# Kernel tuning notes

Hardware: AMD Instinct MI355X
Metric: run time of the kernel (lower is better)

Reference implementation:

```python
import jax, jax.numpy as jnp
import numpy as np

B, N, R = 32768, 9, 4
IN_DIM = 5
DIMS = [64, 128, 256]
BN_EPS = 1e-5
LRELU_SLOPE = 0.2


def _rgcn_block(h, adj, ws, wr, b, gamma, beta):
    # Relational GCN: self transform + per-relation aggregation
    hw = jnp.einsum('bnd,rde->brne', h, wr)        # [B,R,N,D]
    agg = jnp.einsum('brmn,brne->bme', adj, hw)    # [B,N,D]
    h = h @ ws + agg + b
    # BatchNorm1d(max_num_atoms): channel axis is the atom index (training-mode batch stats)
    mean = jnp.mean(h, axis=(0, 2), keepdims=True)
    var = jnp.var(h, axis=(0, 2), keepdims=True)
    h = (h - mean) * jax.lax.rsqrt(var + BN_EPS)
    h = h * gamma[None, :, None] + beta[None, :, None]
    # LeakyReLU(0.2)
    return jnp.where(h > 0, h, LRELU_SLOPE * h)


def setup_inputs() -> dict:
    key = jax.random.key(0)
    ks = jax.random.split(key, 10)
    inp = {
        'atom_feats': jax.random.normal(ks[0], (B, N, IN_DIM), jnp.float32),
        'adj': jax.random.uniform(ks[1], (B, R, N, N), jnp.float32),
        'mask': jnp.ones((B, N), jnp.float32),
    }
    dims = [IN_DIM] + DIMS
    for i in range(3):
        din, dout = dims[i], dims[i + 1]
        inp[f'w_self{i}'] = jax.random.normal(ks[2 + 2 * i], (din, dout), jnp.float32) / np.sqrt(din)
        inp[f'w_rel{i}'] = jax.random.normal(ks[3 + 2 * i], (R, din, dout), jnp.float32) / np.sqrt(din)
        inp[f'b{i}'] = jnp.zeros((dout,), jnp.float32)
        inp[f'g{i}'] = jnp.ones((N,), jnp.float32)
        inp[f'be{i}'] = jnp.zeros((N,), jnp.float32)
    inp['fc_w'] = jax.random.normal(ks[8], (DIMS[-1], 1), jnp.float32) / np.sqrt(DIMS[-1])
    inp['fc_b'] = jnp.zeros((1,), jnp.float32)
    return inp


def reference(atom_feats, adj, mask,
              w_self0, w_rel0, b0, g0, be0,
              w_self1, w_rel1, b1, g1, be1,
              w_self2, w_rel2, b2, g2, be2,
              fc_w, fc_b):
    h = atom_feats
    h = _rgcn_block(h, adj, w_self0, w_rel0, b0, g0, be0)
    h = _rgcn_block(h, adj, w_self1, w_rel1, b1, g1, be1)
    h = _rgcn_block(h, adj, w_self2, w_rel2, b2, g2, be2)
    # masked sum readout
    g = jnp.sum(h * mask[:, :, None], axis=1)   # [B,D]
    out = g @ fc_w + fc_b                        # [B,1]
    return out.squeeze(-1)
```

## Files before the change

### kernel.cpp

```cpp
#include <hip/hip_runtime.h>
#include <hip/hip_bf16.h>


#define NB 32768
#define NA 9
#define NR 4
#define D0 5
#define D1 64
#define D2 128
#define D3 256
#define EPS 1e-5f
#define SLOPE 0.2f
#define NSLOT 64
#define YST 56

typedef __hip_bfloat16 bf16;
typedef short bf16x8 __attribute__((ext_vector_type(8)));
typedef float f32x4 __attribute__((ext_vector_type(4)));
typedef float f32x2 __attribute__((ext_vector_type(2)));

__device__ __forceinline__ float bf2f(bf16 v) { return __bfloat162float(v); }
__device__ __forceinline__ bf16  f2bf(float v) { return __float2bfloat16(v); }

__device__ __forceinline__ void cvt8(bf16x8 v, f32x2 out[4]) {
    union { bf16x8 h; unsigned u[4]; } cv; cv.h = v;
    #pragma unroll
    for (int j = 0; j < 4; j++) {
        out[j].x = __uint_as_float(cv.u[j] << 16);
        out[j].y = __uint_as_float(cv.u[j] & 0xffff0000u);
    }
}

__device__ __forceinline__ bf16x8 pack8(const f32x2 y[4]) {
    union { bf16x8 h; unsigned short s[8]; } cv;
    #pragma unroll
    for (int j = 0; j < 4; j++) {
        union { bf16 b; unsigned short s; } t0, t1;
        t0.b = f2bf(y[j].x); t1.b = f2bf(y[j].y);
        cv.s[2*j] = t0.s; cv.s[2*j+1] = t1.s;
    }
    return cv.h;
}

__global__ __launch_bounds__(256) void k_zero(float* __restrict__ hdr, float* __restrict__ out)
{
    int idx = blockIdx.x * 256 + threadIdx.x;
    if (idx < NB) out[idx] = 0.f;
    if (idx < 6240) hdr[idx] = 0.f;
}

template<int DIN, int DOUT>
__global__ __launch_bounds__(256) void k_prep(const float* __restrict__ ws,
                                              const float* __restrict__ wr,
                                              bf16* __restrict__ wt)
{
    constexpr int K5 = 5*DIN;
    int idx = blockIdx.x*256 + threadIdx.x;
    if (idx >= DOUT*K5) return;
    int n = idx / K5, k = idx % K5;
    int s = k / DIN, kk = k % DIN;
    float v = (s == 0) ? ws[(size_t)kk*DOUT + n]
                       : wr[((size_t)(s-1)*DIN + kk)*DOUT + n];
    wt[idx] = f2bf(v);
}

__global__ __launch_bounds__(256) void k_layer0(
    const float* __restrict__ feats, const float* __restrict__ adj,
    const float* __restrict__ ws, const float* __restrict__ wr,
    const float* __restrict__ bias, bf16* __restrict__ hpre, float* __restrict__ slots)
{
    __shared__ float Wsh[5][5][64];
    __shared__ float Bsh[64];
    __shared__ float Adj[4][4][9][9];
    __shared__ float Hsh[4][9][5];
    __shared__ float bstat[18];

    int tid = threadIdx.x;
    int bl  = tid >> 6;
    int e   = tid & 63;
    int b0  = blockIdx.x * 4;

    for (int i = tid; i < 5*64; i += 256) Wsh[0][i/64][i%64] = ws[i];
    for (int i = tid; i < 4*5*64; i += 256) {
        int s = i / 320, rem = i % 320;
        Wsh[1+s][rem/64][rem%64] = wr[i];
    }
    if (tid < 64) Bsh[tid] = bias[tid];
    if (tid < 18) bstat[tid] = 0.f;
    {
        const float* ap = adj + (size_t)(b0 + bl) * (NR*NA*NA);
        float* dst = &Adj[bl][0][0][0];
        for (int i = e; i < NR*NA*NA; i += 64) dst[i] = ap[i];
    }
    {
        const float* fp = feats + (size_t)(b0 + bl) * (NA*D0);
        float* dst = &Hsh[bl][0][0];
        for (int i = e; i < NA*D0; i += 64) dst[i] = fp[i];
    }
    __syncthreads();

    float X[5][9];
    #pragma unroll
    for (int s = 0; s < 5; s++)
        #pragma unroll
        for (int n = 0; n < 9; n++) {
            float a = 0.f;
            #pragma unroll
            for (int k = 0; k < 5; k++) a += Hsh[bl][n][k] * Wsh[s][k][e];
            X[s][n] = a;
        }
    float bv = Bsh[e];
    float out[9];
    #pragma unroll
    for (int m = 0; m < 9; m++) {
        float a = X[0][m] + bv;
        #pragma unroll
        for (int r = 0; r < 4; r++)
            #pragma unroll
            for (int n = 0; n < 9; n++)
                a += Adj[bl][r][m][n] * X[1+r][n];
        out[m] = a;
    }
    bf16* hp = hpre + (size_t)(b0 + bl) * (NA*D1) + e;
    #pragma unroll
    for (int m = 0; m < 9; m++) hp[m*D1] = f2bf(out[m]);

    #pragma unroll
    for (int m = 0; m < 9; m++) {
        float s = out[m], q = out[m]*out[m];
        #pragma unroll
        for (int off = 32; off > 0; off >>= 1) {
            s += __shfl_xor(s, off, 64);
            q += __shfl_xor(q, off, 64);
        }
        if (e == 0) { atomicAdd(&bstat[m], s); atomicAdd(&bstat[9+m], q); }
    }
    __syncthreads();
    if (tid < 9) {
        float* sl = slots + (size_t)(blockIdx.x & (NSLOT-1)) * 32;
        atomicAdd(&sl[tid],      bstat[tid]);
        atomicAdd(&sl[16+tid],   bstat[9+tid]);
    }
}

template<int DOUT>
__global__ void k_finalize(const float* __restrict__ slots,
                           const float* __restrict__ g, const float* __restrict__ be,
                           float* __restrict__ fin)
{
    int n = threadIdx.x;
    if (n < 9) {
        float s = 0.f, q = 0.f;
        for (int i = 0; i < NSLOT; i++) { s += slots[i*32+n]; q += slots[i*32+16+n]; }
        float cnt = (float)NB * (float)DOUT;
        float mean = s / cnt;
        float var  = q / cnt - mean*mean;
        float sc   = g[n] * rsqrtf(var + EPS);
        fin[n]    = sc;
        fin[16+n] = be[n] - mean * sc;
    }
}

template<int DIN, int DOUT, int MODE>
__global__ __launch_bounds__(256, 3) void k_mfma(
    const bf16*  __restrict__ hprev,
    const float* __restrict__ finPrev,
    const float* __restrict__ adjg,
    const bf16*  __restrict__ wt,
    const float* __restrict__ bias,
    bf16*  __restrict__ hout,
    float* __restrict__ slots,
    const float* __restrict__ finC,
    const float* __restrict__ maskg,
    const float* __restrict__ fcw,
    float* __restrict__ outp)
{
    constexpr int K5 = 5*DIN;
    constexpr int HS = DIN + 8;
    constexpr int NT = DOUT/64;
    constexpr int KS = DIN/32;
    constexpr int HW8 = DIN/8;

    __shared__ __align__(16) bf16 hS[81*HS];
    __shared__ __align__(16) bf16 yS[4*64*YST];
    __shared__ float rstat[128];
    __shared__ float sfinP[32];
    __shared__ float sfinC[32];

    int tid = threadIdx.x;
    int row0 = blockIdx.x * 64;
    int mol_lo = row0 / 9;
    int mol_hi = (row0 + 63) / 9;
    int nmol = mol_hi - mol_lo + 1;
    int off = row0 - mol_lo*9;

    if (tid < 32) sfinP[tid] = finPrev[tid];
    if constexpr (MODE == 2) { if (tid >= 32 && tid < 64) sfinC[tid-32] = finC[tid-32]; }
    if (tid >= 64 && tid < 192) rstat[tid-64] = 0.f;

    int brow = tid >> 2;
    int bc8  = (tid & 3) * 8;
    int bloc = off + brow;
    int bml  = bloc / 9;
    int ba   = bloc - bml*9;
    float adjR[4][9];
    {
        const float* ap = adjg + (size_t)(mol_lo + bml)*324 + ba*9;
        #pragma unroll
        for (int r = 0; r < 4; r++)
            #pragma unroll
            for (int n = 0; n < 9; n++) adjR[r][n] = ap[r*81 + n];
    }
    __syncthreads();

    for (int i = tid; i < nmol*9*HW8; i += 256) {
        int rl = i / HW8;
        int a  = rl % 9;
        int c8 = (i % HW8)*8;
        bf16x8 hv = *(const bf16x8*)(hprev + (size_t)(mol_lo*9 + rl)*DIN + c8);
        f32x2 hf[4]; cvt8(hv, hf);
        float sc = sfinP[a], sh = sfinP[16+a];
        f32x2 o[4];
        #pragma unroll
        for (int j = 0; j < 4; j++) {
            float v0 = sc*hf[j].x + sh; v0 = fmaxf(v0, SLOPE*v0);
            float v1 = sc*hf[j].y + sh; v1 = fmaxf(v1, SLOPE*v1);
            o[j] = (f32x2){v0, v1};
        }
        *(bf16x8*)(&hS[rl*HS + c8]) = pack8(o);
    }
    __syncthreads();

    int wv = tid >> 6, lane = tid & 63;
    int q = lane >> 4, l15 = lane & 15;

    f32x4 acc[4][NT];
    #pragma unroll
    for (int mt = 0; mt < 4; mt++)
        #pragma unroll
        for (int t = 0; t < NT; t++) acc[mt][t] = (f32x4){0.f, 0.f, 0.f, 0.f};

    const bf16* wp[NT];
    #pragma unroll
    for (int t = 0; t < NT; t++)
        wp[t] = wt + (size_t)((wv*NT + t)*16 + l15)*K5 + q*8;

    #pragma unroll
    for (int ks = 0; ks < KS; ks++) {
        bf16x8 Af[4], Bf[NT];
        #pragma unroll
        for (int mt = 0; mt < 4; mt++)
            Af[mt] = *(const bf16x8*)(hS + (size_t)(off + mt*16 + l15)*HS + ks*32 + q*8);
        #pragma unroll
        for (int t = 0; t < NT; t++)
            Bf[t] = *(const bf16x8*)(wp[t] + ks*32);
        #pragma unroll
        for (int mt = 0; mt < 4; mt++)
            #pragma unroll
            for (int t = 0; t < NT; t++)
                acc[mt][t] = __builtin_amdgcn_mfma_f32_16x16x32_bf16(Af[mt], Bf[t], acc[mt][t], 0, 0, 0);
    }

    for (int kc = 0; kc < KS; kc++) {
        {
            const bf16* hb = hS + (size_t)(bml*9)*HS + kc*32 + bc8;
            f32x2 y[4][4];
            #pragma unroll
            for (int r = 0; r < 4; r++)
                #pragma unroll
                for (int j = 0; j < 4; j++) y[r][j] = (f32x2){0.f, 0.f};
            #pragma unroll
            for (int n = 0; n < 9; n++) {
                bf16x8 hv = *(const bf16x8*)(hb + n*HS);
                f32x2 hf[4]; cvt8(hv, hf);
                #pragma unroll
                for (int r = 0; r < 4; r++) {
                    f32x2 av = (f32x2){adjR[r][n], adjR[r][n]};
                    #pragma unroll
                    for (int j = 0; j < 4; j++)
                        y[r][j] = __builtin_elementwise_fma(av, hf[j], y[r][j]);
                }
            }
            #pragma unroll
            for (int r = 0; r < 4; r++)
                *(bf16x8*)(&yS[(r*64 + brow)*YST + bc8]) = pack8(y[r]);
        }
        __syncthreads();
        #pragma unroll
        for (int r = 0; r < 4; r++) {
            int kcol = DIN + (r*KS + kc)*32;
            bf16x8 Af[4], Bf[NT];
            #pragma unroll
            for (int mt = 0; mt < 4; mt++)
                Af[mt] = *(const bf16x8*)(&yS[(r*64 + mt*16 + l15)*YST + q*8]);
            #pragma unroll
            for (int t = 0; t < NT; t++)
                Bf[t] = *(const bf16x8*)(wp[t] + kcol);
            #pragma unroll
            for (int mt = 0; mt < 4; mt++)
                #pragma unroll
                for (int t = 0; t < NT; t++)
                    acc[mt][t] = __builtin_amdgcn_mfma_f32_16x16x32_bf16(Af[mt], Bf[t], acc[mt][t], 0, 0, 0);
        }
        __syncthreads();
    }

    float bcol[NT];
    #pragma unroll
    for (int t = 0; t < NT; t++) bcol[t] = bias[(wv*NT + t)*16 + l15];

    if constexpr (MODE == 2) {
        float fwv[NT];
        #pragma unroll
        for (int t = 0; t < NT; t++) fwv[t] = fcw[(wv*NT + t)*16 + l15];
        #pragma unroll
        for (int mt = 0; mt < 4; mt++) {
            #pragma unroll
            for (int reg = 0; reg < 4; reg++) {
                int rloc = mt*16 + q*4 + reg;
                int atom = (row0 + rloc) % 9;
                float sc = sfinC[atom], sh = sfinC[16+atom];
                float part = 0.f;
                #pragma unroll
                for (int t = 0; t < NT; t++) {
                    float v = acc[mt][t][reg] + bcol[t];
                    float y = sc*v + sh;
                    y = fmaxf(y, SLOPE*y);
                    part += y * fwv[t];
                }
                part += __shfl_xor(part, 1); part += __shfl_xor(part, 2);
                part += __shfl_xor(part, 4); part += __shfl_xor(part, 8);
                if (l15 == 0) atomicAdd(&rstat[rloc], part);
            }
        }
        __syncthreads();
        if (tid < 64) {
            int rg = row0 + tid;
            int b = rg / 9;
            atomicAdd(&outp[b], rstat[tid] * maskg[rg]);
        }
        return;
    }

    #pragma unroll
    for (int mt = 0; mt < 4; mt++) {
        #pragma unroll
        for (int reg = 0; reg < 4; reg++) {
            int rloc = mt*16 + q*4 + reg;
            float s = 0.f, qq = 0.f;
            #pragma unroll
            for (int t = 0; t < NT; t++) {
                float v = acc[mt][t][reg] + bcol[t];
                if constexpr (MODE == 0) {
                    size_t o = (size_t)(row0 + rloc)*DOUT + (wv*NT + t)*16 + l15;
                    hout[o] = f2bf(v);
                }
                s += v; qq += v*v;
            }
            s += __shfl_xor(s, 1); s += __shfl_xor(s, 2);
            s += __shfl_xor(s, 4); s += __shfl_xor(s, 8);
            qq += __shfl_xor(qq, 1); qq += __shfl_xor(qq, 2);
            qq += __shfl_xor(qq, 4); qq += __shfl_xor(qq, 8);
            if (l15 == 0) { atomicAdd(&rstat[rloc*2], s); atomicAdd(&rstat[rloc*2+1], qq); }
        }
    }
    __syncthreads();
    if (tid < 64) {
        int rg = row0 + tid;
        int atom = rg % 9;
        float* sl = slots + (size_t)(blockIdx.x & (NSLOT-1))*32;
        atomicAdd(&sl[atom],    rstat[tid*2]);
        atomicAdd(&sl[16+atom], rstat[tid*2+1]);
    }
}

__global__ __launch_bounds__(256) void k_readout(
    const bf16* __restrict__ h2, const float* __restrict__ fin,
    const float* __restrict__ mask, const float* __restrict__ fcw,
    const float* __restrict__ fcb, float* __restrict__ out)
{
    int tid = threadIdx.x;
    int w = tid >> 6, lane = tid & 63;
    int b = blockIdx.x * 4 + w;
    float sc[9], sh[9];
    #pragma unroll
    for (int n = 0; n < 9; n++) { sc[n] = fin[n]; sh[n] = fin[16+n]; }
    const bf16* hp = h2 + (size_t)b * (NA*D3) + lane*4;
    float acc0 = 0.f, acc1 = 0.f, acc2 = 0.f, acc3 = 0.f;
    #pragma unroll
    for (int n = 0; n < 9; n++) {
        bf16 v4[4] __attribute__((aligned(8)));
        *(uint2*)v4 = *(const uint2*)(hp + n*D3);
        float mk = mask[(size_t)b*NA + n];
        float v;
        v = sc[n]*bf2f(v4[0]) + sh[n]; v = fmaxf(v, SLOPE*v); acc0 += v*mk;
        v = sc[n]*bf2f(v4[1]) + sh[n]; v = fmaxf(v, SLOPE*v); acc1 += v*mk;
        v = sc[n]*bf2f(v4[2]) + sh[n]; v = fmaxf(v, SLOPE*v); acc2 += v*mk;
        v = sc[n]*bf2f(v4[3]) + sh[n]; v = fmaxf(v, SLOPE*v); acc3 += v*mk;
    }
    float4 wv = *(const float4*)(fcw + lane*4);
    float s = acc0*wv.x + acc1*wv.y + acc2*wv.z + acc3*wv.w;
    #pragma unroll
    for (int off = 1; off < 64; off <<= 1) s += __shfl_xor(s, off, 64);
    if (lane == 0) out[b] = s + fcb[0];
}

__global__ __launch_bounds__(256) void k_addfcb(float* __restrict__ out, const float* __restrict__ fcb)
{
    int idx = blockIdx.x * 256 + threadIdx.x;
    if (idx < NB) out[idx] += fcb[0];
}


extern "C" void kernel_launch(void* const* d_in, const int* in_sizes, int n_in,
                              void* d_out, int out_size, void* d_ws, size_t ws_size,
                              hipStream_t stream)
{
    const float* feats = (const float*)d_in[0];
    const float* adj   = (const float*)d_in[1];
    const float* mask  = (const float*)d_in[2];
    const float* ws0 = (const float*)d_in[3];
    const float* wr0 = (const float*)d_in[4];
    const float* b0  = (const float*)d_in[5];
    const float* g0  = (const float*)d_in[6];
    const float* be0 = (const float*)d_in[7];
    const float* ws1 = (const float*)d_in[8];
    const float* wr1 = (const float*)d_in[9];
    const float* b1  = (const float*)d_in[10];
    const float* g1  = (const float*)d_in[11];
    const float* be1 = (const float*)d_in[12];
    const float* ws2 = (const float*)d_in[13];
    const float* wr2 = (const float*)d_in[14];
    const float* b2  = (const float*)d_in[15];
    const float* g2  = (const float*)d_in[16];
    const float* be2 = (const float*)d_in[17];
    const float* fcw = (const float*)d_in[18];
    const float* fcb = (const float*)d_in[19];
    float* outp = (float*)d_out;

    char* wsb = (char*)d_ws;
    float* slots0 = (float*)(wsb + 0);
    float* slots1 = slots0 + NSLOT*32;
    float* slots2 = slots1 + NSLOT*32;
    float* fin0 = (float*)(wsb + 24576);
    float* fin1 = fin0 + 32;
    float* fin2 = fin1 + 32;
    bf16* wt1 = (bf16*)(wsb + 32768);
    bf16* wt2 = (bf16*)(wsb + 114688);

    k_zero<<<(NB+255)/256, 256, 0, stream>>>((float*)wsb, outp);
    k_prep<D1, D2><<<(D2*5*D1 + 255)/256, 256, 0, stream>>>(ws1, wr1, wt1);
    k_prep<D2, D3><<<(D3*5*D2 + 255)/256, 256, 0, stream>>>(ws2, wr2, wt2);

    bool bigws = (ws_size >= 227016704ULL);
    const int GRID = (NB*NA)/64;

    if (bigws) {
        bf16* h1 = (bf16*)(wsb + 524288ULL);
        bf16* h2 = (bf16*)(wsb + 76021760ULL);
        bf16* h0 = h2;

        k_layer0<<<NB/4, 256, 0, stream>>>(feats, adj, ws0, wr0, b0, h0, slots0);
        k_finalize<D1><<<1, 64, 0, stream>>>(slots0, g0, be0, fin0);

        k_mfma<D1, D2, 0><<<GRID, 256, 0, stream>>>(
            h0, fin0, adj, wt1, b1, h1, slots1, nullptr, nullptr, nullptr, nullptr);
        k_finalize<D2><<<1, 64, 0, stream>>>(slots1, g1, be1, fin1);

        k_mfma<D2, D3, 0><<<GRID, 256, 0, stream>>>(
            h1, fin1, adj, wt2, b2, h2, slots2, nullptr, nullptr, nullptr, nullptr);
        k_finalize<D3><<<1, 64, 0, stream>>>(slots2, g2, be2, fin2);

        k_readout<<<NB/4, 256, 0, stream>>>(h2, fin2, mask, fcw, fcb, outp);
    } else {
        bf16* h0 = (bf16*)(wsb + 524288ULL);
        bf16* h1 = (bf16*)(wsb + 38273024ULL);

        k_layer0<<<NB/4, 256, 0, stream>>>(feats, adj, ws0, wr0, b0, h0, slots0);
        k_finalize<D1><<<1, 64, 0, stream>>>(slots0, g0, be0, fin0);

        k_mfma<D1, D2, 0><<<GRID, 256, 0, stream>>>(
            h0, fin0, adj, wt1, b1, h1, slots1, nullptr, nullptr, nullptr, nullptr);
        k_finalize<D2><<<1, 64, 0, stream>>>(slots1, g1, be1, fin1);

        k_mfma<D2, D3, 1><<<GRID, 256, 0, stream>>>(
            h1, fin1, adj, wt2, b2, nullptr, slots2, nullptr, nullptr, nullptr, nullptr);
        k_finalize<D3><<<1, 64, 0, stream>>>(slots2, g2, be2, fin2);

        k_mfma<D2, D3, 2><<<GRID, 256, 0, stream>>>(
            h1, fin1, adj, wt2, b2, nullptr, nullptr, fin2, mask, fcw, outp);
        k_addfcb<<<(NB+255)/256, 256, 0, stream>>>(outp, fcb);
    }
}
```

Measured before the change: 704.4 us.

## Reorder RGCN layers to transform-then-aggregate with MFMA adjacency and deterministic stats

The fused layer kernel now computes H·W_s and H·W_r for every relation with MFMA first, then aggregates per molecule with a second MFMA against a padded bf16 adjacency tile. Blocks cover 5 molecules and a 64-column output slice on a 2D grid, so atom rows are aligned to molecule boundaries. BatchNorm statistics move out of atomics into separate k_stats / finalize2 reduction kernels, and the readout writes per-column-block partials that are summed afterwards. This removes atomic contention and the scalar adjacency FMA pass, at the cost of redundant adjacency staging per column block, extra passes over activations for stats, and lower occupancy.

```diff
diff --git a/kernel.cpp b/kernel.cpp
--- a/kernel.cpp
+++ b/kernel.cpp
@@ -11,8 +11,9 @@
 #define D3 256
 #define EPS 1e-5f
 #define SLOPE 0.2f
-#define NSLOT 64
-#define YST 56
+#define NMOL 5
+#define MR 48
+#define NBLK ((NB + NMOL - 1) / NMOL)
 
 typedef __hip_bfloat16 bf16;
 typedef short bf16x8 __attribute__((ext_vector_type(8)));
@@ -21,6 +22,9 @@
 
 __device__ __forceinline__ float bf2f(bf16 v) { return __bfloat162float(v); }
 __device__ __forceinline__ bf16  f2bf(float v) { return __float2bfloat16(v); }
+__device__ __forceinline__ short f2bfs(float v) {
+    union { bf16 b; short s; } u; u.b = __float2bfloat16(v); return u.s;
+}
 
 __device__ __forceinline__ void cvt8(bf16x8 v, f32x2 out[4]) {
     union { bf16x8 h; unsigned u[4]; } cv; cv.h = v;
@@ -42,38 +46,30 @@
     return cv.h;
 }
 
-__global__ __launch_bounds__(256) void k_zero(float* __restrict__ hdr, float* __restrict__ out)
-{
-    int idx = blockIdx.x * 256 + threadIdx.x;
-    if (idx < NB) out[idx] = 0.f;
-    if (idx < 6240) hdr[idx] = 0.f;
-}
-
 template<int DIN, int DOUT>
 __global__ __launch_bounds__(256) void k_prep(const float* __restrict__ ws,
                                               const float* __restrict__ wr,
                                               bf16* __restrict__ wt)
 {
-    constexpr int K5 = 5*DIN;
     int idx = blockIdx.x*256 + threadIdx.x;
-    if (idx >= DOUT*K5) return;
-    int n = idx / K5, k = idx % K5;
-    int s = k / DIN, kk = k % DIN;
-    float v = (s == 0) ? ws[(size_t)kk*DOUT + n]
-                       : wr[((size_t)(s-1)*DIN + kk)*DOUT + n];
+    if (idx >= 5*DOUT*DIN) return;
+    int s = idx / (DOUT*DIN);
+    int rem = idx % (DOUT*DIN);
+    int n = rem / DIN, k = rem % DIN;
+    float v = (s == 0) ? ws[(size_t)k*DOUT + n]
+                       : wr[((size_t)(s-1)*DIN + k)*DOUT + n];
     wt[idx] = f2bf(v);
 }
 
 __global__ __launch_bounds__(256) void k_layer0(
     const float* __restrict__ feats, const float* __restrict__ adj,
     const float* __restrict__ ws, const float* __restrict__ wr,
-    const float* __restrict__ bias, bf16* __restrict__ hpre, float* __restrict__ slots)
+    const float* __restrict__ bias, bf16* __restrict__ hpre)
 {
     __shared__ float Wsh[5][5][64];
     __shared__ float Bsh[64];
     __shared__ float Adj[4][4][9][9];
     __shared__ float Hsh[4][9][5];
-    __shared__ float bstat[18];
 
     int tid = threadIdx.x;
     int bl  = tid >> 6;
@@ -86,7 +82,6 @@
         Wsh[1+s][rem/64][rem%64] = wr[i];
     }
     if (tid < 64) Bsh[tid] = bias[tid];
-    if (tid < 18) bstat[tid] = 0.f;
     {
         const float* ap = adj + (size_t)(b0 + bl) * (NR*NA*NA);
         float* dst = &Adj[bl][0][0][0];
@@ -110,7 +105,7 @@
             X[s][n] = a;
         }
     float bv = Bsh[e];
-    float out[9];
+    bf16* hp = hpre + (size_t)(b0 + bl) * (NA*D1) + e;
     #pragma unroll
     for (int m = 0; m < 9; m++) {
         float a = X[0][m] + bv;
@@ -119,39 +114,52 @@
             #pragma unroll
             for (int n = 0; n < 9; n++)
                 a += Adj[bl][r][m][n] * X[1+r][n];
-        out[m] = a;
-    }
-    bf16* hp = hpre + (size_t)(b0 + bl) * (NA*D1) + e;
-    #pragma unroll
-    for (int m = 0; m < 9; m++) hp[m*D1] = f2bf(out[m]);
-
-    #pragma unroll
-    for (int m = 0; m < 9; m++) {
-        float s = out[m], q = out[m]*out[m];
-        #pragma unroll
-        for (int off = 32; off > 0; off >>= 1) {
-            s += __shfl_xor(s, off, 64);
-            q += __shfl_xor(q, off, 64);
-        }
-        if (e == 0) { atomicAdd(&bstat[m], s); atomicAdd(&bstat[9+m], q); }
-    }
+        hp[m*D1] = f2bf(a);
+    }
+}
+
+template<int D>
+__global__ __launch_bounds__(256) void k_stats(const bf16* __restrict__ h,
+                                               float2* __restrict__ sbuf)
+{
+    int g = blockIdx.x;
+    int a = blockIdx.y;
+    int tid = threadIdx.x;
+    constexpr int NIT = (512*D/8)/256;
+    const bf16* base = h + ((size_t)g*512*NA + a)*D;
+    float s = 0.f, q = 0.f;
+    for (int it = 0; it < NIT; it++) {
+        int i = (it*256 + tid)*8;
+        int b = i / D, c = i % D;
+        bf16x8 hv = *(const bf16x8*)(base + (size_t)b*NA*D + c);
+        f32x2 hf[4]; cvt8(hv, hf);
+        #pragma unroll
+        for (int j = 0; j < 4; j++) {
+            s += hf[j].x + hf[j].y;
+            q += hf[j].x*hf[j].x + hf[j].y*hf[j].y;
+        }
+    }
+    #pragma unroll
+    for (int off = 1; off < 64; off <<= 1) {
+        s += __shfl_xor(s, off, 64);
+        q += __shfl_xor(q, off, 64);
+    }
+    __shared__ float ls[4], lq[4];
+    if ((tid & 63) == 0) { ls[tid >> 6] = s; lq[tid >> 6] = q; }
     __syncthreads();
-    if (tid < 9) {
-        float* sl = slots + (size_t)(blockIdx.x & (NSLOT-1)) * 32;
-        atomicAdd(&sl[tid],      bstat[tid]);
-        atomicAdd(&sl[16+tid],   bstat[9+tid]);
-    }
+    if (tid == 0)
+        sbuf[a*64 + g] = (float2){ls[0]+ls[1]+ls[2]+ls[3], lq[0]+lq[1]+lq[2]+lq[3]};
 }
 
 template<int DOUT>
-__global__ void k_finalize(const float* __restrict__ slots,
+__global__ void k_finalize(const float2* __restrict__ sbuf,
                            const float* __restrict__ g, const float* __restrict__ be,
                            float* __restrict__ fin)
 {
     int n = threadIdx.x;
     if (n < 9) {
         float s = 0.f, q = 0.f;
-        for (int i = 0; i < NSLOT; i++) { s += slots[i*32+n]; q += slots[i*32+16+n]; }
+        for (int i = 0; i < 64; i++) { float2 v = sbuf[n*64 + i]; s += v.x; q += v.y; }
         float cnt = (float)NB * (float)DOUT;
         float mean = s / cnt;
         float var  = q / cnt - mean*mean;
@@ -161,216 +169,279 @@
     }
 }
 
+__global__ __launch_bounds__(256) void k_finalize2(
+    const float* __restrict__ pbS, const float* __restrict__ pbQ,
+    const float* __restrict__ g, const float* __restrict__ be, float* __restrict__ fin)
+{
+    int a = blockIdx.x;
+    int tid = threadIdx.x;
+    float s = 0.f, q = 0.f;
+    for (int i = tid; i < NBLK*4; i += 256) { s += pbS[(size_t)i*16 + a]; q += pbQ[(size_t)i*16 + a]; }
+    #pragma unroll
+    for (int off = 1; off < 64; off <<= 1) {
+        s += __shfl_xor(s, off, 64);
+        q += __shfl_xor(q, off, 64);
+    }
+    __shared__ float ls[4], lq[4];
+    if ((tid & 63) == 0) { ls[tid >> 6] = s; lq[tid >> 6] = q; }
+    __syncthreads();
+    if (tid == 0) {
+        float S = ls[0]+ls[1]+ls[2]+ls[3];
+        float Q = lq[0]+lq[1]+lq[2]+lq[3];
+        float cnt = (float)NB * (float)D3;
+        float mean = S / cnt;
+        float var  = Q / cnt - mean*mean;
+        float sc   = g[a] * rsqrtf(var + EPS);
+        fin[a]    = sc;
+        fin[16+a] = be[a] - mean * sc;
+    }
+}
+
 template<int DIN, int DOUT, int MODE>
-__global__ __launch_bounds__(256, 3) void k_mfma(
+__global__ __launch_bounds__(256, 2) void k_fused(
     const bf16*  __restrict__ hprev,
     const float* __restrict__ finPrev,
     const float* __restrict__ adjg,
     const bf16*  __restrict__ wt,
     const float* __restrict__ bias,
     bf16*  __restrict__ hout,
-    float* __restrict__ slots,
+    float* __restrict__ pbS,
+    float* __restrict__ pbQ,
     const float* __restrict__ finC,
     const float* __restrict__ maskg,
     const float* __restrict__ fcw,
-    float* __restrict__ outp)
-{
-    constexpr int K5 = 5*DIN;
-    constexpr int HS = DIN + 8;
-    constexpr int NT = DOUT/64;
-    constexpr int KS = DIN/32;
+    float* __restrict__ out4)
+{
+    constexpr int HSP = DIN + 8;
+    constexpr int SRP = 80;
+    constexpr int XTP = 4*SRP + 8;
+    constexpr int AP  = 72;
+    constexpr int KK1 = DIN/32;
     constexpr int HW8 = DIN/8;
 
-    __shared__ __align__(16) bf16 hS[81*HS];
-    __shared__ __align__(16) bf16 yS[4*64*YST];
-    __shared__ float rstat[128];
+    __shared__ __align__(16) bf16  hS[MR*HSP];
+    __shared__ __align__(16) short xT[64*XTP];
+    __shared__ __align__(16) bf16  adjB[NMOL*16*AP];
+    __shared__ float aggL[64*45];
+    __shared__ float wsumS[4*48], wsumQ[4*48];
+    __shared__ float rowS[48], rowQ[48];
     __shared__ float sfinP[32];
-    __shared__ float sfinC[32];
+    __shared__ float sfinC2[32];
 
     int tid = threadIdx.x;
-    int row0 = blockIdx.x * 64;
-    int mol_lo = row0 / 9;
-    int mol_hi = (row0 + 63) / 9;
-    int nmol = mol_hi - mol_lo + 1;
-    int off = row0 - mol_lo*9;
-
-    if (tid < 32) sfinP[tid] = finPrev[tid];
-    if constexpr (MODE == 2) { if (tid >= 32 && tid < 64) sfinC[tid-32] = finC[tid-32]; }
-    if (tid >= 64 && tid < 192) rstat[tid-64] = 0.f;
-
-    int brow = tid >> 2;
-    int bc8  = (tid & 3) * 8;
-    int bloc = off + brow;
-    int bml  = bloc / 9;
-    int ba   = bloc - bml*9;
-    float adjR[4][9];
-    {
-        const float* ap = adjg + (size_t)(mol_lo + bml)*324 + ba*9;
-        #pragma unroll
-        for (int r = 0; r < 4; r++)
-            #pragma unroll
-            for (int n = 0; n < 9; n++) adjR[r][n] = ap[r*81 + n];
+    int lane = tid & 63;
+    int wv = tid >> 6;
+    int mol_lo = blockIdx.x * NMOL;
+    int nmol = NB - mol_lo; if (nmol > NMOL) nmol = NMOL;
+    int nrow = nmol * 9;
+    int cb = blockIdx.y * 64;
+
+    if (lane < 32) sfinP[lane] = finPrev[lane];
+    if constexpr (MODE == 2) { if (lane >= 32) sfinC2[lane-32] = finC[lane-32]; }
+
+    const bf16x8 z8 = (bf16x8){0,0,0,0,0,0,0,0};
+
+    for (int i = tid; i < 64*XTP/8; i += 256) ((bf16x8*)xT)[i] = z8;
+
+    for (int i = tid; i < MR*HW8; i += 256) {
+        int rl = i / HW8;
+        int c8 = (i % HW8)*8;
+        bf16x8 o8 = z8;
+        if (rl < nrow) {
+            bf16x8 hv = *(const bf16x8*)(hprev + (size_t)(mol_lo*9 + rl)*DIN + c8);
+            f32x2 hf[4]; cvt8(hv, hf);
+            int a = rl % 9;
+            float sc = sfinP[a], sh = sfinP[16+a];
+            f32x2 o[4];
+            #pragma unroll
+            for (int j = 0; j < 4; j++) {
+                float v0 = sc*hf[j].x + sh; v0 = fmaxf(v0, SLOPE*v0);
+                float v1 = sc*hf[j].y + sh; v1 = fmaxf(v1, SLOPE*v1);
+                o[j] = (f32x2){v0, v1};
+            }
+            o8 = pack8(o);
+        }
+        *(bf16x8*)(&hS[rl*HSP + c8]) = o8;
+    }
+
+    for (int i = tid; i < NMOL*7*(AP/8); i += 256) {
+        int molm = i / (AP/8);
+        int c8 = (i % (AP/8))*8;
+        int mol = molm / 7, m = 9 + molm % 7;
+        *(bf16x8*)(&adjB[(mol*16 + m)*AP + c8]) = z8;
+    }
+    for (int i = tid; i < NMOL*9*4*7; i += 256) {
+        int mol = i / 252;
+        int t = i % 252;
+        int m = t / 28;
+        int u = t % 28;
+        int r = u / 7, n = 9 + u % 7;
+        adjB[(mol*16 + m)*AP + 16*r + n] = f2bf(0.f);
+    }
+    for (int i = tid; i < nmol*324; i += 256) {
+        int mol = i / 324;
+        int t = i % 324;
+        int r = t / 81;
+        int m = (t % 81) / 9;
+        int n = t % 9;
+        float v = adjg[(size_t)(mol_lo + mol)*324 + t];
+        adjB[(mol*16 + m)*AP + 16*r + n] = f2bf(v);
     }
     __syncthreads();
 
-    for (int i = tid; i < nmol*9*HW8; i += 256) {
-        int rl = i / HW8;
-        int a  = rl % 9;
-        int c8 = (i % HW8)*8;
-        bf16x8 hv = *(const bf16x8*)(hprev + (size_t)(mol_lo*9 + rl)*DIN + c8);
-        f32x2 hf[4]; cvt8(hv, hf);
-        float sc = sfinP[a], sh = sfinP[16+a];
-        f32x2 o[4];
-        #pragma unroll
-        for (int j = 0; j < 4; j++) {
-            float v0 = sc*hf[j].x + sh; v0 = fmaxf(v0, SLOPE*v0);
-            float v1 = sc*hf[j].y + sh; v1 = fmaxf(v1, SLOPE*v1);
-            o[j] = (f32x2){v0, v1};
-        }
-        *(bf16x8*)(&hS[rl*HS + c8]) = pack8(o);
-    }
-    __syncthreads();
-
-    int wv = tid >> 6, lane = tid & 63;
     int q = lane >> 4, l15 = lane & 15;
-
-    f32x4 acc[4][NT];
-    #pragma unroll
-    for (int mt = 0; mt < 4; mt++)
-        #pragma unroll
-        for (int t = 0; t < NT; t++) acc[mt][t] = (f32x4){0.f, 0.f, 0.f, 0.f};
-
-    const bf16* wp[NT];
-    #pragma unroll
-    for (int t = 0; t < NT; t++)
-        wp[t] = wt + (size_t)((wv*NT + t)*16 + l15)*K5 + q*8;
-
-    #pragma unroll
-    for (int ks = 0; ks < KS; ks++) {
-        bf16x8 Af[4], Bf[NT];
-        #pragma unroll
-        for (int mt = 0; mt < 4; mt++)
-            Af[mt] = *(const bf16x8*)(hS + (size_t)(off + mt*16 + l15)*HS + ks*32 + q*8);
-        #pragma unroll
-        for (int t = 0; t < NT; t++)
-            Bf[t] = *(const bf16x8*)(wp[t] + ks*32);
-        #pragma unroll
-        for (int mt = 0; mt < 4; mt++)
-            #pragma unroll
-            for (int t = 0; t < NT; t++)
-                acc[mt][t] = __builtin_amdgcn_mfma_f32_16x16x32_bf16(Af[mt], Bf[t], acc[mt][t], 0, 0, 0);
-    }
-
-    for (int kc = 0; kc < KS; kc++) {
+    int wl = wv*16 + l15;
+    int wcol = cb + wl;
+
+    f32x4 accS[3];
+    f32x4 accR[4][3];
+    #pragma unroll
+    for (int mt = 0; mt < 3; mt++) accS[mt] = (f32x4){0.f,0.f,0.f,0.f};
+    #pragma unroll
+    for (int s = 0; s < 4; s++)
+        #pragma unroll
+        for (int mt = 0; mt < 3; mt++) accR[s][mt] = (f32x4){0.f,0.f,0.f,0.f};
+
+    const bf16* wbase = wt + (size_t)wcol*DIN + q*8;
+    #pragma unroll
+    for (int kk = 0; kk < KK1; kk++) {
+        bf16x8 Af[3];
+        #pragma unroll
+        for (int mt = 0; mt < 3; mt++)
+            Af[mt] = *(const bf16x8*)(&hS[(mt*16 + l15)*HSP + kk*32 + q*8]);
         {
-            const bf16* hb = hS + (size_t)(bml*9)*HS + kc*32 + bc8;
-            f32x2 y[4][4];
-            #pragma unroll
-            for (int r = 0; r < 4; r++)
-                #pragma unroll
-                for (int j = 0; j < 4; j++) y[r][j] = (f32x2){0.f, 0.f};
-            #pragma unroll
-            for (int n = 0; n < 9; n++) {
-                bf16x8 hv = *(const bf16x8*)(hb + n*HS);
-                f32x2 hf[4]; cvt8(hv, hf);
-                #pragma unroll
-                for (int r = 0; r < 4; r++) {
-                    f32x2 av = (f32x2){adjR[r][n], adjR[r][n]};
-                    #pragma unroll
-                    for (int j = 0; j < 4; j++)
-                        y[r][j] = __builtin_elementwise_fma(av, hf[j], y[r][j]);
+            bf16x8 Bf = *(const bf16x8*)(wbase + kk*32);
+            #pragma unroll
+            for (int mt = 0; mt < 3; mt++)
+                accS[mt] = __builtin_amdgcn_mfma_f32_16x16x32_bf16(Af[mt], Bf, accS[mt], 0, 0, 0);
+        }
+        #pragma unroll
+        for (int s = 0; s < 4; s++) {
+            bf16x8 Bf = *(const bf16x8*)(wbase + (size_t)(s+1)*DOUT*DIN + kk*32);
+            #pragma unroll
+            for (int mt = 0; mt < 3; mt++)
+                accR[s][mt] = __builtin_amdgcn_mfma_f32_16x16x32_bf16(Af[mt], Bf, accR[s][mt], 0, 0, 0);
+        }
+    }
+    short* xcol = xT + (size_t)wl*XTP;
+    #pragma unroll
+    for (int s = 0; s < 4; s++)
+        #pragma unroll
+        for (int mt = 0; mt < 3; mt++)
+            #pragma unroll
+            for (int reg = 0; reg < 4; reg++) {
+                int row = mt*16 + q*4 + reg;
+                if (row < 45) {
+                    int mu = row / 9, n = row % 9;
+                    xcol[s*SRP + mu*16 + n] = f2bfs(accR[s][mt][reg]);
                 }
             }
-            #pragma unroll
-            for (int r = 0; r < 4; r++)
-                *(bf16x8*)(&yS[(r*64 + brow)*YST + bc8]) = pack8(y[r]);
+
+    f32x4 accA[NMOL];
+    for (int mu = 0; mu < nmol; mu++) {
+        f32x4 acc = (f32x4){0.f,0.f,0.f,0.f};
+        #pragma unroll
+        for (int kk = 0; kk < 2; kk++) {
+            int k0 = kk*32 + q*8;
+            int rr = k0 >> 4;
+            int n0 = k0 & 15;
+            bf16x8 Af = *(const bf16x8*)(&adjB[((mu*16) + l15)*AP + k0]);
+            bf16x8 Bf = *(const bf16x8*)(&xcol[rr*SRP + mu*16 + n0]);
+            acc = __builtin_amdgcn_mfma_f32_16x16x32_bf16(Af, Bf, acc, 0, 0, 0);
+        }
+        accA[mu] = acc;
+    }
+    for (int mu = 0; mu < nmol; mu++) {
+        #pragma unroll
+        for (int reg = 0; reg < 4; reg++) {
+            int atom = q*4 + reg;
+            if (atom < 9) aggL[wl*45 + mu*9 + atom] = accA[mu][reg];
+        }
+    }
+
+    float bcol = bias[wcol];
+
+    if constexpr (MODE == 0) {
+        #pragma unroll
+        for (int mt = 0; mt < 3; mt++) {
+            #pragma unroll
+            for (int reg = 0; reg < 4; reg++) {
+                int row = mt*16 + q*4 + reg;
+                if (row < nrow) {
+                    float v = accS[mt][reg] + aggL[wl*45 + row] + bcol;
+                    hout[(size_t)(mol_lo*9 + row)*DOUT + wcol] = f2bf(v);
+                }
+            }
+        }
+        return;
+    }
+
+    if constexpr (MODE == 1) {
+        #pragma unroll
+        for (int mt = 0; mt < 3; mt++) {
+            #pragma unroll
+            for (int reg = 0; reg < 4; reg++) {
+                int row = mt*16 + q*4 + reg;
+                float s = 0.f, qq = 0.f;
+                if (row < nrow) {
+                    float v = accS[mt][reg] + aggL[wl*45 + row] + bcol;
+                    s = v; qq = v*v;
+                }
+                s += __shfl_xor(s, 1); s += __shfl_xor(s, 2);
+                s += __shfl_xor(s, 4); s += __shfl_xor(s, 8);
+                qq += __shfl_xor(qq, 1); qq += __shfl_xor(qq, 2);
+                qq += __shfl_xor(qq, 4); qq += __shfl_xor(qq, 8);
+                if (l15 == 0) { wsumS[wv*48 + row] = s; wsumQ[wv*48 + row] = qq; }
+            }
         }
         __syncthreads();
-        #pragma unroll
-        for (int r = 0; r < 4; r++) {
-            int kcol = DIN + (r*KS + kc)*32;
-            bf16x8 Af[4], Bf[NT];
-            #pragma unroll
-            for (int mt = 0; mt < 4; mt++)
-                Af[mt] = *(const bf16x8*)(&yS[(r*64 + mt*16 + l15)*YST + q*8]);
-            #pragma unroll
-            for (int t = 0; t < NT; t++)
-                Bf[t] = *(const bf16x8*)(wp[t] + kcol);
-            #pragma unroll
-            for (int mt = 0; mt < 4; mt++)
-                #pragma unroll
-                for (int t = 0; t < NT; t++)
-                    acc[mt][t] = __builtin_amdgcn_mfma_f32_16x16x32_bf16(Af[mt], Bf[t], acc[mt][t], 0, 0, 0);
+        if (tid < 48) {
+            rowS[tid] = wsumS[tid] + wsumS[48+tid] + wsumS[96+tid] + wsumS[144+tid];
+            rowQ[tid] = wsumQ[tid] + wsumQ[48+tid] + wsumQ[96+tid] + wsumQ[144+tid];
         }
         __syncthreads();
-    }
-
-    float bcol[NT];
-    #pragma unroll
-    for (int t = 0; t < NT; t++) bcol[t] = bias[(wv*NT + t)*16 + l15];
-
-    if constexpr (MODE == 2) {
-        float fwv[NT];
-        #pragma unroll
-        for (int t = 0; t < NT; t++) fwv[t] = fcw[(wv*NT + t)*16 + l15];
-        #pragma unroll
-        for (int mt = 0; mt < 4; mt++) {
+        if (tid < 9) {
+            float sA = 0.f, qA = 0.f;
+            #pragma unroll
+            for (int mu = 0; mu < NMOL; mu++) { sA += rowS[mu*9 + tid]; qA += rowQ[mu*9 + tid]; }
+            size_t pi = ((size_t)blockIdx.y*NBLK + blockIdx.x)*16 + tid;
+            pbS[pi] = sA;
+            pbQ[pi] = qA;
+        }
+        return;
+    }
+
+    {
+        float fw = fcw[wcol];
+        #pragma unroll
+        for (int mt = 0; mt < 3; mt++) {
             #pragma unroll
             for (int reg = 0; reg < 4; reg++) {
-                int rloc = mt*16 + q*4 + reg;
-                int atom = (row0 + rloc) % 9;
-                float sc = sfinC[atom], sh = sfinC[16+atom];
+                int row = mt*16 + q*4 + reg;
                 float part = 0.f;
-                #pragma unroll
-                for (int t = 0; t < NT; t++) {
-                    float v = acc[mt][t][reg] + bcol[t];
-                    float y = sc*v + sh;
+                if (row < nrow) {
+                    int atom = row % 9;
+                    float v = accS[mt][reg] + aggL[wl*45 + row] + bcol;
+                    float y = sfinC2[atom]*v + sfinC2[16+atom];
                     y = fmaxf(y, SLOPE*y);
-                    part += y * fwv[t];
+                    part = y * fw;
                 }
                 part += __shfl_xor(part, 1); part += __shfl_xor(part, 2);
                 part += __shfl_xor(part, 4); part += __shfl_xor(part, 8);
-                if (l15 == 0) atomicAdd(&rstat[rloc], part);
+                if (l15 == 0) wsumS[wv*48 + row] = part;
             }
         }
         __syncthreads();
-        if (tid < 64) {
-            int rg = row0 + tid;
-            int b = rg / 9;
-            atomicAdd(&outp[b], rstat[tid] * maskg[rg]);
-        }
-        return;
-    }
-
-    #pragma unroll
-    for (int mt = 0; mt < 4; mt++) {
-        #pragma unroll
-        for (int reg = 0; reg < 4; reg++) {
-            int rloc = mt*16 + q*4 + reg;
-            float s = 0.f, qq = 0.f;
-            #pragma unroll
-            for (int t = 0; t < NT; t++) {
-                float v = acc[mt][t][reg] + bcol[t];
-                if constexpr (MODE == 0) {
-                    size_t o = (size_t)(row0 + rloc)*DOUT + (wv*NT + t)*16 + l15;
-                    hout[o] = f2bf(v);
-                }
-                s += v; qq += v*v;
-            }
-            s += __shfl_xor(s, 1); s += __shfl_xor(s, 2);
-            s += __shfl_xor(s, 4); s += __shfl_xor(s, 8);
-            qq += __shfl_xor(qq, 1); qq += __shfl_xor(qq, 2);
-            qq += __shfl_xor(qq, 4); qq += __shfl_xor(qq, 8);
-            if (l15 == 0) { atomicAdd(&rstat[rloc*2], s); atomicAdd(&rstat[rloc*2+1], qq); }
-        }
-    }
-    __syncthreads();
-    if (tid < 64) {
-        int rg = row0 + tid;
-        int atom = rg % 9;
-        float* sl = slots + (size_t)(blockIdx.x & (NSLOT-1))*32;
-        atomicAdd(&sl[atom],    rstat[tid*2]);
-        atomicAdd(&sl[16+atom], rstat[tid*2+1]);
+        if (tid < nrow)
+            rowS[tid] = (wsumS[tid] + wsumS[48+tid] + wsumS[96+tid] + wsumS[144+tid])
+                        * maskg[(size_t)mol_lo*9 + tid];
+        __syncthreads();
+        if (tid < nmol) {
+            float t = 0.f;
+            #pragma unroll
+            for (int j = 0; j < 9; j++) t += rowS[tid*9 + j];
+            out4[(size_t)blockIdx.y*NB + mol_lo + tid] = t;
+        }
     }
 }
 
@@ -398,17 +469,20 @@
         v = sc[n]*bf2f(v4[2]) + sh[n]; v = fmaxf(v, SLOPE*v); acc2 += v*mk;
         v = sc[n]*bf2f(v4[3]) + sh[n]; v = fmaxf(v, SLOPE*v); acc3 += v*mk;
     }
-    float4 wv = *(const float4*)(fcw + lane*4);
-    float s = acc0*wv.x + acc1*wv.y + acc2*wv.z + acc3*wv.w;
+    float4 wvv = *(const float4*)(fcw + lane*4);
+    float s = acc0*wvv.x + acc1*wvv.y + acc2*wvv.z + acc3*wvv.w;
     #pragma unroll
     for (int off = 1; off < 64; off <<= 1) s += __shfl_xor(s, off, 64);
     if (lane == 0) out[b] = s + fcb[0];
 }
 
-__global__ __launch_bounds__(256) void k_addfcb(float* __restrict__ out, const float* __restrict__ fcb)
+__global__ __launch_bounds__(256) void k_sum4(float* __restrict__ out,
+                                              const float* __restrict__ out4,
+                                              const float* __restrict__ fcb)
 {
     int idx = blockIdx.x * 256 + threadIdx.x;
-    if (idx < NB) out[idx] += fcb[0];
+    if (idx < NB)
+        out[idx] = out4[idx] + out4[NB+idx] + out4[2*NB+idx] + out4[3*NB+idx] + fcb[0];
 }
 
 
@@ -439,56 +513,65 @@
     float* outp = (float*)d_out;
 
     char* wsb = (char*)d_ws;
-    float* slots0 = (float*)(wsb + 0);
-    float* slots1 = slots0 + NSLOT*32;
-    float* slots2 = slots1 + NSLOT*32;
-    float* fin0 = (float*)(wsb + 24576);
+    float2* sbuf0 = (float2*)(wsb + 0);
+    float2* sbuf1 = sbuf0 + 576;
+    float2* sbuf2 = sbuf1 + 576;
+    float* fin0 = (float*)(wsb + 16384);
     float* fin1 = fin0 + 32;
     float* fin2 = fin1 + 32;
     bf16* wt1 = (bf16*)(wsb + 32768);
     bf16* wt2 = (bf16*)(wsb + 114688);
-
-    k_zero<<<(NB+255)/256, 256, 0, stream>>>((float*)wsb, outp);
-    k_prep<D1, D2><<<(D2*5*D1 + 255)/256, 256, 0, stream>>>(ws1, wr1, wt1);
-    k_prep<D2, D3><<<(D3*5*D2 + 255)/256, 256, 0, stream>>>(ws2, wr2, wt2);
-
-    bool bigws = (ws_size >= 227016704ULL);
-    const int GRID = (NB*NA)/64;
+    float* out4 = (float*)(wsb + 442368);
+    float* pbS  = (float*)(wsb + 966656);
+    float* pbQ  = (float*)(wsb + 2644480);
+
+    k_prep<D1, D2><<<(5*D2*D1 + 255)/256, 256, 0, stream>>>(ws1, wr1, wt1);
+    k_prep<D2, D3><<<(5*D3*D2 + 255)/256, 256, 0, stream>>>(ws2, wr2, wt2);
+
+    bool bigws = (ws_size >= 231211008ULL);
+    dim3 sgrid(64, 9);
+    dim3 g1d(NBLK, D2/64);
+    dim3 g2d(NBLK, D3/64);
 
     if (bigws) {
-        bf16* h1 = (bf16*)(wsb + 524288ULL);
-        bf16* h2 = (bf16*)(wsb + 76021760ULL);
+        bf16* h1 = (bf16*)(wsb + 4718592ULL);
+        bf16* h2 = (bf16*)(wsb + 80216064ULL);
         bf16* h0 = h2;
 
-        k_layer0<<<NB/4, 256, 0, stream>>>(feats, adj, ws0, wr0, b0, h0, slots0);
-        k_finalize<D1><<<1, 64, 0, stream>>>(slots0, g0, be0, fin0);
-
-        k_mfma<D1, D2, 0><<<GRID, 256, 0, stream>>>(
-            h0, fin0, adj, wt1, b1, h1, slots1, nullptr, nullptr, nullptr, nullptr);
-        k_finalize<D2><<<1, 64, 0, stream>>>(slots1, g1, be1, fin1);
-
-        k_mfma<D2, D3, 0><<<GRID, 256, 0, stream>>>(
-            h1, fin1, adj, wt2, b2, h2, slots2, nullptr, nullptr, nullptr, nullptr);
-        k_finalize<D3><<<1, 64, 0, stream>>>(slots2, g2, be2, fin2);
+        k_layer0<<<NB/4, 256, 0, stream>>>(feats, adj, ws0, wr0, b0, h0);
+        k_stats<D1><<<sgrid, 256, 0, stream>>>(h0, sbuf0);
+        k_finalize<D1><<<1, 64, 0, stream>>>(sbuf0, g0, be0, fin0);
+
+        k_fused<D1, D2, 0><<<g1d, 256, 0, stream>>>(
+            h0, fin0, adj, wt1, b1, h1, nullptr, nullptr, nullptr, nullptr, nullptr, nullptr);
+        k_stats<D2><<<sgrid, 256, 0, stream>>>(h1, sbuf1);
+        k_finalize<D2><<<1, 64, 0, stream>>>(sbuf1, g1, be1, fin1);
+
+        k_fused<D2, D3, 0><<<g2d, 256, 0, stream>>>(
+            h1, fin1, adj, wt2, b2, h2, nullptr, nullptr, nullptr, nullptr, nullptr, nullptr);
+        k_stats<D3><<<sgrid, 256, 0, stream>>>(h2, sbuf2);
+        k_finalize<D3><<<1, 64, 0, stream>>>(sbuf2, g2, be2, fin2);
 
         k_readout<<<NB/4, 256, 0, stream>>>(h2, fin2, mask, fcw, fcb, outp);
     } else {
-        bf16* h0 = (bf16*)(wsb + 524288ULL);
-        bf16* h1 = (bf16*)(wsb + 38273024ULL);
-
-        k_layer0<<<NB/4, 256, 0, stream>>>(feats, adj, ws0, wr0, b0, h0, slots0);
-        k_finalize<D1><<<1, 64, 0, stream>>>(slots0, g0, be0, fin0);
-
-        k_mfma<D1, D2, 0><<<GRID, 256, 0, stream>>>(
-            h0, fin0, adj, wt1, b1, h1, slots1, nullptr, nullptr, nullptr, nullptr);
-        k_finalize<D2><<<1, 64, 0, stream>>>(slots1, g1, be1, fin1);
-
-        k_mfma<D2, D3, 1><<<GRID, 256, 0, stream>>>(
-            h1, fin1, adj, wt2, b2, nullptr, slots2, nullptr, nullptr, nullptr, nullptr);
-        k_finalize<D3><<<1, 64, 0, stream>>>(slots2, g2, be2, fin2);
-
-        k_mfma<D2, D3, 2><<<GRID, 256, 0, stream>>>(
-            h1, fin1, adj, wt2, b2, nullptr, nullptr, fin2, mask, fcw, outp);
-        k_addfcb<<<(NB+255)/256, 256, 0, stream>>>(outp, fcb);
-    }
-}
+        bf16* h0 = (bf16*)(wsb + 4718592ULL);
+        bf16* h1 = (bf16*)(wsb + 42467328ULL);
+
+        k_layer0<<<NB/4, 256, 0, stream>>>(feats, adj, ws0, wr0, b0, h0);
+        k_stats<D1><<<sgrid, 256, 0, stream>>>(h0, sbuf0);
+        k_finalize<D1><<<1, 64, 0, stream>>>(sbuf0, g0, be0, fin0);
+
+        k_fused<D1, D2, 0><<<g1d, 256, 0, stream>>>(
+            h0, fin0, adj, wt1, b1, h1, nullptr, nullptr, nullptr, nullptr, nullptr, nullptr);
+        k_stats<D2><<<sgrid, 256, 0, stream>>>(h1, sbuf1);
+        k_finalize<D2><<<1, 64, 0, stream>>>(sbuf1, g1, be1, fin1);
+
+        k_fused<D2, D3, 1><<<g2d, 256, 0, stream>>>(
+            h1, fin1, adj, wt2, b2, nullptr, pbS, pbQ, nullptr, nullptr, nullptr, nullptr);
+        k_finalize2<<<9, 256, 0, stream>>>(pbS, pbQ, g2, be2, fin2);
+
+        k_fused<D2, D3, 2><<<g2d, 256, 0, stream>>>(
+            h1, fin1, adj, wt2, b2, nullptr, nullptr, nullptr, fin2, mask, fcw, out4);
+        k_sum4<<<(NB+255)/256, 256, 0, stream>>>(outp, out4, fcb);
+    }
+}
```

New measurement: 1.118 ms. +58.8%, slower.
